# Kernel optimization log

Hardware: AMD Instinct MI355X
Metric: run time of the kernel (lower is better)

Reference implementation:

```python
import jax, jax.numpy as jnp
import numpy as np

D = 1024
H = 16
DH = D // H

def setup_inputs() -> dict:
    key = jax.random.key(0)
    ks = jax.random.split(key, 9)
    s = 0.02
    return {
        "x": jax.random.normal(ks[0], (2, 2048, D), dtype=jnp.float32),
        "Wq": jax.random.normal(ks[1], (D, D), dtype=jnp.float32) * s,
        "bq": jnp.zeros((D,), dtype=jnp.float32),
        "Wk": jax.random.normal(ks[2], (D, D), dtype=jnp.float32) * s,
        "bk": jnp.zeros((D,), dtype=jnp.float32),
        "Wv": jax.random.normal(ks[3], (D, D), dtype=jnp.float32) * s,
        "bv": jnp.zeros((D,), dtype=jnp.float32),
        "Wo": jax.random.normal(ks[4], (D, D), dtype=jnp.float32) * s,
        "bo": jnp.zeros((D,), dtype=jnp.float32),
    }

def reference(x, Wq, bq, Wk, bk, Wv, bv, Wo, bo):
    B, S, Dm = x.shape
    def proj(W, b):
        # [B,S,D] -> [B,H,S,DH]
        return (x @ W + b).reshape(B, S, H, DH).transpose(0, 2, 1, 3)
    q = proj(Wq, bq)
    k = proj(Wk, bk)
    v = proj(Wv, bv)
    scale = 1.0 / np.sqrt(DH).astype(np.float32)
    raw = jnp.einsum('bhsd,bhtd->bhst', q, k) * scale  # [B,H,S,S]
    w = jax.nn.softmax(raw, axis=-1)
    out = jnp.einsum('bhst,bhtd->bhsd', w, v)          # [B,H,S,DH]
    out = out.transpose(0, 2, 1, 3).reshape(B, S, Dm)
    return out @ Wo + bo
```

## Files before the change

### kernel.cpp

```cpp
#include <hip/hip_runtime.h>
#include <math.h>

constexpr int Dm  = 1024;
constexpr int NH  = 16;
constexpr int SQ  = 2048;
constexpr int NB  = 2;

typedef float f32x4 __attribute__((ext_vector_type(4)));
typedef float f32x16 __attribute__((ext_vector_type(16)));
typedef short bf16x8 __attribute__((ext_vector_type(8)));
typedef __attribute__((address_space(3))) unsigned int lds_u32;
typedef __attribute__((address_space(1))) const unsigned int glb_u32;

__device__ __forceinline__ void gload_lds16(const void* g, void* l) {
    __builtin_amdgcn_global_load_lds((glb_u32*)(uintptr_t)g, (lds_u32*)(uintptr_t)l, 16, 0, 0);
}

__device__ __forceinline__ unsigned short bf_round(float x) {
    unsigned u = __float_as_uint(x);
    unsigned r = u + 0x7fffu + ((u >> 16) & 1u);
    return (unsigned short)(r >> 16);
}

__device__ __forceinline__ float exp2_fast(float x) {
    float r;
    asm("v_exp_f32 %0, %1" : "=v"(r) : "v"(x));
    return r;
}

__device__ __forceinline__ unsigned cvt_pk(float lo, float hi_) {
    unsigned r;
    asm("v_cvt_pk_bf16_f32 %0, %1, %2" : "=v"(r) : "v"(lo), "v"(hi_));
    return r;
}

__device__ __forceinline__ void permlane_swap(unsigned& a, unsigned& b) {
    asm volatile("v_permlane32_swap_b32 %0, %1" : "+v"(a), "+v"(b));
}

__device__ __forceinline__ bf16x8 make_frag(unsigned a, unsigned b, unsigned c, unsigned d) {
    union { unsigned u[4]; bf16x8 v; } uu;
    uu.u[0] = a; uu.u[1] = b; uu.u[2] = c; uu.u[3] = d;
    return uu.v;
}

__global__ __launch_bounds__(256) void prologue(const float* __restrict__ x,
                                                const float* __restrict__ Wq,
                                                const float* __restrict__ Wk,
                                                const float* __restrict__ Wv,
                                                const float* __restrict__ Wo,
                                                unsigned short* __restrict__ xb,
                                                unsigned short* __restrict__ wt) {
    const int z = blockIdx.z;
    const int tid = threadIdx.x;
    if (z == 4) {
        size_t base = ((size_t)blockIdx.y * 16 + blockIdx.x) * 16384;
#pragma unroll
        for (int it = 0; it < 8; ++it) {
            size_t i = base + (size_t)it * 2048 + (size_t)tid * 8;
            float4 a = *(const float4*)&x[i];
            float4 b = *(const float4*)&x[i + 4];
            unsigned short o8[8] __attribute__((aligned(16)));
            o8[0] = bf_round(a.x); o8[1] = bf_round(a.y); o8[2] = bf_round(a.z); o8[3] = bf_round(a.w);
            o8[4] = bf_round(b.x); o8[5] = bf_round(b.y); o8[6] = bf_round(b.z); o8[7] = bf_round(b.w);
            *(uint4*)&xb[i] = *(const uint4*)o8;
        }
        return;
    }
    const float* W = (z == 0) ? Wq : (z == 1) ? Wk : (z == 2) ? Wv : Wo;
    unsigned short* dst = wt + (size_t)z * Dm * Dm;
    __shared__ float T[64][65];
    const int k0 = blockIdx.x * 64, n0 = blockIdx.y * 64;
#pragma unroll
    for (int i = 0; i < 4; ++i) {
        int s = tid + i * 256;
        int kk = s >> 4, c = (s & 15) * 4;
        *(float4*)&T[kk][c] = *(const float4*)&W[(size_t)(k0 + kk) * Dm + n0 + c];
    }
    __syncthreads();
#pragma unroll
    for (int i = 0; i < 2; ++i) {
        int s = tid + i * 256;
        int n = s >> 3, c8 = (s & 7) * 8;
        unsigned short o8[8] __attribute__((aligned(16)));
#pragma unroll
        for (int j = 0; j < 8; ++j) o8[j] = bf_round(T[c8 + j][n]);
        *(uint4*)&dst[(size_t)(n0 + n) * Dm + k0 + c8] = *(const uint4*)o8;
    }
}

__global__ __launch_bounds__(512) void gemm_qkv192(
    const unsigned short* __restrict__ xb,
    const unsigned short* __restrict__ wt,
    const float* __restrict__ bq, const float* __restrict__ bk,
    const float* __restrict__ bv,
    unsigned short* __restrict__ qbuf, unsigned short* __restrict__ kbuf,
    unsigned short* __restrict__ vtbuf)
{
    __shared__ unsigned short Alds[2][256 * 64];
    __shared__ unsigned short Blds[2][192 * 64];

    const int tid = threadIdx.x;
    const int lane = tid & 63, wid = tid >> 6;
    const int wm = wid >> 2, wn = wid & 3;
    const int l15 = lane & 15, lg = lane >> 4;

    const int bid = blockIdx.x;
    const int swz = (bid & 7) * 32 + (bid >> 3);
    const int bx = swz & 15, by = swz >> 4;
    const int m0 = by * 256, n0 = bx * 192;

    const int srow = wid * 8 + (lane >> 3);
    const int scol = ((lane & 7) ^ ((lane >> 3) & 7)) * 8;

    const unsigned short* Abase = xb + (size_t)m0 * Dm;
    const unsigned short* Bbase = wt + (size_t)n0 * Dm;

#define STAGE_TILE(t)                                                              \
    do {                                                                           \
        const unsigned short* As_ = Abase + (t) * 64;                              \
        const unsigned short* Bs_ = Bbase + (t) * 64;                              \
        unsigned short* Ad_ = Alds[(t) & 1];                                       \
        unsigned short* Bd_ = Blds[(t) & 1];                                       \
        _Pragma("unroll")                                                          \
        for (int i_ = 0; i_ < 4; ++i_)                                             \
            gload_lds16(&As_[(size_t)(i_ * 64 + srow) * Dm + scol],                \
                        &Ad_[i_ * 4096 + wid * 512]);                              \
        _Pragma("unroll")                                                          \
        for (int i_ = 0; i_ < 3; ++i_)                                             \
            gload_lds16(&Bs_[(size_t)(i_ * 64 + srow) * Dm + scol],                \
                        &Bd_[i_ * 4096 + wid * 512]);                              \
    } while (0)

    f32x4 acc[8][3];
#pragma unroll
    for (int mr = 0; mr < 8; ++mr)
#pragma unroll
        for (int nr = 0; nr < 3; ++nr) acc[mr][nr] = (f32x4){0.f, 0.f, 0.f, 0.f};

    STAGE_TILE(0);
    asm volatile("s_waitcnt vmcnt(0)" ::: "memory");
    __builtin_amdgcn_s_barrier();

    for (int t = 0; t < Dm / 64; ++t) {
        unsigned short* Ad = Alds[t & 1];
        unsigned short* Bd = Blds[t & 1];
        if (t + 1 < Dm / 64) STAGE_TILE(t + 1);

        bf16x8 a_[4][2], b_[3][2];

#define RD_A(qm, fr, ks) \
    (*(const bf16x8*)&Ad[(wm * 128 + (qm) * 64 + (fr) * 16 + l15) * 64 + \
                         ((((ks) * 4 + lg) ^ (l15 & 7)) * 8)])
#define RD_B(fc, ks) \
    (*(const bf16x8*)&Bd[(wn * 48 + (fc) * 16 + l15) * 64 + \
                         ((((ks) * 4 + lg) ^ (l15 & 7)) * 8)])

#pragma unroll
        for (int fr = 0; fr < 4; ++fr) {
            a_[fr][0] = RD_A(0, fr, 0); a_[fr][1] = RD_A(0, fr, 1);
        }
#pragma unroll
        for (int fc = 0; fc < 3; ++fc) {
            b_[fc][0] = RD_B(fc, 0); b_[fc][1] = RD_B(fc, 1);
        }
        __builtin_amdgcn_s_barrier();
        __builtin_amdgcn_s_setprio(1);
#pragma unroll
        for (int fr = 0; fr < 4; ++fr)
#pragma unroll
            for (int fc = 0; fc < 3; ++fc)
#pragma unroll
                for (int ks = 0; ks < 2; ++ks)
                    acc[fr][fc] = __builtin_amdgcn_mfma_f32_16x16x32_bf16(
                        a_[fr][ks], b_[fc][ks], acc[fr][fc], 0, 0, 0);
        __builtin_amdgcn_s_setprio(0);
        __builtin_amdgcn_s_barrier();

#pragma unroll
        for (int fr = 0; fr < 4; ++fr) {
            a_[fr][0] = RD_A(1, fr, 0); a_[fr][1] = RD_A(1, fr, 1);
        }
        __builtin_amdgcn_s_barrier();
        __builtin_amdgcn_s_setprio(1);
#pragma unroll
        for (int fr = 0; fr < 4; ++fr)
#pragma unroll
            for (int fc = 0; fc < 3; ++fc)
#pragma unroll
                for (int ks = 0; ks < 2; ++ks)
                    acc[4 + fr][fc] = __builtin_amdgcn_mfma_f32_16x16x32_bf16(
                        a_[fr][ks], b_[fc][ks], acc[4 + fr][fc], 0, 0, 0);
        __builtin_amdgcn_s_setprio(0);
        __builtin_amdgcn_s_barrier();

        asm volatile("s_waitcnt vmcnt(0)" ::: "memory");
        __builtin_amdgcn_s_barrier();
#undef RD_A
#undef RD_B
    }

    const float qscale = 0.18033688011f;
#pragma unroll
    for (int mr = 0; mr < 8; ++mr) {
#pragma unroll
        for (int nr = 0; nr < 3; ++nr) {
            const int m = m0 + wm * 128 + mr * 16 + lg * 4;
            const int nglob = n0 + wn * 48 + nr * 16 + l15;
            const int zq = nglob >> 10;
            const int nz = nglob & 1023;
            const float* bias = (zq == 0) ? bq : (zq == 1) ? bk : bv;
            const float bb_ = bias[nz];
            if (zq == 0) {
#pragma unroll
                for (int rr = 0; rr < 4; ++rr)
                    qbuf[(size_t)(m + rr) * Dm + nz] =
                        bf_round((acc[mr][nr][rr] + bb_) * qscale);
            } else if (zq == 1) {
#pragma unroll
                for (int rr = 0; rr < 4; ++rr)
                    kbuf[(size_t)(m + rr) * Dm + nz] = bf_round(acc[mr][nr][rr] + bb_);
            } else {
                const int bbv = m >> 11, s = m & (SQ - 1);
                const int hh = nz >> 6, d = nz & 63;
                unsigned short p4[4] __attribute__((aligned(8)));
#pragma unroll
                for (int rr = 0; rr < 4; ++rr) p4[rr] = bf_round(acc[mr][nr][rr] + bb_);
                *(uint2*)&vtbuf[(((size_t)bbv * NH + hh) * 64 + d) * SQ + s] =
                    *(const uint2*)p4;
            }
        }
    }
#undef STAGE_TILE
}

__global__ __launch_bounds__(256) void gemm_out8(const unsigned short* __restrict__ A,
                                                 const unsigned short* __restrict__ Bt,
                                                 const float* __restrict__ bias,
                                                 float* __restrict__ Cf) {
    __shared__ unsigned short Alds[2][128 * 64];
    __shared__ unsigned short Blds[2][128 * 64];

    const int tid = threadIdx.x;
    const int lane = tid & 63, wid = tid >> 6;
    const int l15 = lane & 15, lg = lane >> 4;
    const int wr = (wid >> 1) * 64, wc = (wid & 1) * 64;
    const int m0 = blockIdx.y * 128, n0 = blockIdx.x * 128;

    const int srow = (tid >> 3) & 31;
    const int scol = ((tid & 7) ^ (srow & 7)) * 8;

    const unsigned short* Abase = A + (size_t)m0 * Dm;
    const unsigned short* Bbase = Bt + (size_t)n0 * Dm;

#define STAGE_TILE(t)                                                              \
    do {                                                                           \
        const unsigned short* As_ = Abase + (t) * 64;                              \
        const unsigned short* Bs_ = Bbase + (t) * 64;                              \
        unsigned short* Ad_ = Alds[(t) & 1];                                       \
        unsigned short* Bd_ = Blds[(t) & 1];                                       \
        _Pragma("unroll")                                                          \
        for (int i_ = 0; i_ < 4; ++i_) {                                           \
            gload_lds16(&As_[(size_t)(i_ * 32 + srow) * Dm + scol],                \
                        &Ad_[i_ * 2048 + wid * 512]);                              \
            gload_lds16(&Bs_[(size_t)(i_ * 32 + srow) * Dm + scol],                \
                        &Bd_[i_ * 2048 + wid * 512]);                              \
        }                                                                          \
    } while (0)

    f32x4 acc[4][4];
#pragma unroll
    for (int r = 0; r < 4; ++r)
#pragma unroll
        for (int c = 0; c < 4; ++c) acc[r][c] = (f32x4){0.f, 0.f, 0.f, 0.f};

    STAGE_TILE(0);
    asm volatile("s_waitcnt vmcnt(0)" ::: "memory");
    __builtin_amdgcn_s_barrier();

    for (int t = 0; t < Dm / 64; ++t) {
        unsigned short* Ad = Alds[t & 1];
        unsigned short* Bd = Blds[t & 1];
        if (t + 1 < Dm / 64) STAGE_TILE(t + 1);

        bf16x8 a_[4][2], b_[2][2];

#define RD_A(fr, ks) \
    (*(const bf16x8*)&Ad[(wr + (fr) * 16 + l15) * 64 + ((((ks) * 4 + lg) ^ (l15 & 7)) * 8)])
#define RD_B(fc, ks) \
    (*(const bf16x8*)&Bd[(wc + (fc) * 16 + l15) * 64 + ((((ks) * 4 + lg) ^ (l15 & 7)) * 8)])

#pragma unroll
        for (int fr = 0; fr < 4; ++fr) {
            a_[fr][0] = RD_A(fr, 0); a_[fr][1] = RD_A(fr, 1);
        }
#pragma unroll
        for (int fc = 0; fc < 2; ++fc) {
            b_[fc][0] = RD_B(fc, 0); b_[fc][1] = RD_B(fc, 1);
        }
        __builtin_amdgcn_s_barrier();
        __builtin_amdgcn_s_setprio(1);
#pragma unroll
        for (int fr = 0; fr < 4; ++fr)
#pragma unroll
            for (int fc = 0; fc < 2; ++fc)
#pragma unroll
                for (int ks = 0; ks < 2; ++ks)
                    acc[fr][fc] = __builtin_amdgcn_mfma_f32_16x16x32_bf16(
                        a_[fr][ks], b_[fc][ks], acc[fr][fc], 0, 0, 0);
        __builtin_amdgcn_s_setprio(0);
        __builtin_amdgcn_s_barrier();

#pragma unroll
        for (int fc = 0; fc < 2; ++fc) {
            b_[fc][0] = RD_B(2 + fc, 0); b_[fc][1] = RD_B(2 + fc, 1);
        }
        __builtin_amdgcn_s_barrier();
        __builtin_amdgcn_s_setprio(1);
#pragma unroll
        for (int fr = 0; fr < 4; ++fr)
#pragma unroll
            for (int fc = 0; fc < 2; ++fc)
#pragma unroll
                for (int ks = 0; ks < 2; ++ks)
                    acc[fr][2 + fc] = __builtin_amdgcn_mfma_f32_16x16x32_bf16(
                        a_[fr][ks], b_[fc][ks], acc[fr][2 + fc], 0, 0, 0);
        __builtin_amdgcn_s_setprio(0);
        __builtin_amdgcn_s_barrier();

        asm volatile("s_waitcnt vmcnt(0)" ::: "memory");
        __builtin_amdgcn_s_barrier();
#undef RD_A
#undef RD_B
    }

#pragma unroll
    for (int r = 0; r < 4; ++r) {
#pragma unroll
        for (int c = 0; c < 4; ++c) {
            const int mBase = m0 + wr + r * 16 + lg * 4;
            const int n = n0 + wc + c * 16 + l15;
            const float bv_ = bias[n];
#pragma unroll
            for (int rr = 0; rr < 4; ++rr)
                Cf[(size_t)(mBase + rr) * Dm + n] = acc[r][c][rr] + bv_;
        }
    }
#undef STAGE_TILE
}

__global__ __launch_bounds__(256) void attn_bf16(const unsigned short* q,
                                                 const unsigned short* __restrict__ k,
                                                 const unsigned short* __restrict__ vt,
                                                 unsigned short* ao) {
    __shared__ unsigned short KVs[2][2][64 * 64];
    const int qt = blockIdx.x, h = blockIdx.y, b = blockIdx.z;
    const int tid = threadIdx.x, lane = tid & 63, wid = tid >> 6;
    const int l31 = lane & 31, hi = lane >> 5;

    const size_t qrow0 = (size_t)b * SQ + qt * 128;
    const unsigned short* qp = q + (qrow0 + wid * 32 + l31) * Dm + h * 64;
    bf16x8 qf[4];
#pragma unroll
    for (int ks = 0; ks < 4; ++ks)
        qf[ks] = *(const bf16x8*)&qp[ks * 16 + hi * 8];

    const unsigned short* kb = k + (size_t)b * SQ * Dm + h * 64;
    const unsigned short* vb = vt + ((size_t)b * NH + h) * 64 * SQ;

    const int row0 = tid >> 3;
    const int s8 = (tid & 7) * 8;
    const int sw8 = (((tid & 7) ^ (row0 & 7))) * 8;
    const int koff0 = row0 * 64 + sw8;
    const int koff1 = (row0 + 32) * 64 + sw8;

    {
        uint4 k0v = *(const uint4*)&kb[(size_t)row0 * Dm + s8];
        uint4 k1v = *(const uint4*)&kb[(size_t)(row0 + 32) * Dm + s8];
        uint4 v0v = *(const uint4*)&vb[(size_t)row0 * SQ + s8];
        uint4 v1v = *(const uint4*)&vb[(size_t)(row0 + 32) * SQ + s8];
        *(uint4*)&KVs[0][0][koff0] = k0v; *(uint4*)&KVs[0][0][koff1] = k1v;
        *(uint4*)&KVs[0][1][koff0] = v0v; *(uint4*)&KVs[0][1][koff1] = v1v;
    }
    __syncthreads();

    float psum = 0.f;
    f32x16 c0, c1;
#pragma unroll
    for (int i = 0; i < 16; ++i) { c0[i] = 0.f; c1[i] = 0.f; }

    int cur = 0;
    for (int t0 = 0; t0 < SQ; t0 += 64) {
        const bool hasNext = (t0 + 64) < SQ;
        uint4 kr0, kr1, vr0, vr1;
        if (hasNext) {
            const unsigned short* kn = kb + (size_t)(t0 + 64) * Dm;
            const unsigned short* vn = vb + (t0 + 64);
            kr0 = *(const uint4*)&kn[(size_t)row0 * Dm + s8];
            kr1 = *(const uint4*)&kn[(size_t)(row0 + 32) * Dm + s8];
            vr0 = *(const uint4*)&vn[(size_t)row0 * SQ + s8];
            vr1 = *(const uint4*)&vn[(size_t)(row0 + 32) * SQ + s8];
        }
        const unsigned short* Kc = KVs[cur][0];
        const unsigned short* Vc = KVs[cur][1];

#pragma unroll
        for (int kblk = 0; kblk < 2; ++kblk) {
            f32x16 p;
#pragma unroll
            for (int i = 0; i < 16; ++i) p[i] = 0.f;
            __builtin_amdgcn_s_setprio(1);
#pragma unroll
            for (int ks = 0; ks < 4; ++ks) {
                int row = kblk * 32 + l31;
                int slot = ((ks * 2 + hi) ^ (l31 & 7)) * 8;
                bf16x8 kf = *(const bf16x8*)&Kc[row * 64 + slot];
                p = __builtin_amdgcn_mfma_f32_32x32x16_bf16(kf, qf[ks], p, 0, 0, 0);
            }
            __builtin_amdgcn_s_setprio(0);

            float e[16];
#pragma unroll
            for (int i = 0; i < 16; ++i) { e[i] = exp2_fast(p[i]); psum += e[i]; }
            unsigned w0 = cvt_pk(e[0], e[1]),   w1 = cvt_pk(e[2], e[3]);
            unsigned w2 = cvt_pk(e[4], e[5]),   w3 = cvt_pk(e[6], e[7]);
            unsigned w4 = cvt_pk(e[8], e[9]),   w5 = cvt_pk(e[10], e[11]);
            unsigned w6 = cvt_pk(e[12], e[13]), w7 = cvt_pk(e[14], e[15]);
            permlane_swap(w0, w2); permlane_swap(w1, w3);
            permlane_swap(w4, w6); permlane_swap(w5, w7);
            bf16x8 pf0 = make_frag(w0, w1, w2, w3);
            bf16x8 pf1 = make_frag(w4, w5, w6, w7);

            int s0 = ((kblk * 4 + hi) ^ (l31 & 7)) * 8;
            int s1 = ((kblk * 4 + 2 + hi) ^ (l31 & 7)) * 8;
            bf16x8 va0 = *(const bf16x8*)&Vc[l31 * 64 + s0];
            bf16x8 va1 = *(const bf16x8*)&Vc[l31 * 64 + s1];
            bf16x8 vb0 = *(const bf16x8*)&Vc[(32 + l31) * 64 + s0];
            bf16x8 vb1 = *(const bf16x8*)&Vc[(32 + l31) * 64 + s1];
            __builtin_amdgcn_s_setprio(1);
            c0 = __builtin_amdgcn_mfma_f32_32x32x16_bf16(va0, pf0, c0, 0, 0, 0);
            c0 = __builtin_amdgcn_mfma_f32_32x32x16_bf16(va1, pf1, c0, 0, 0, 0);
            c1 = __builtin_amdgcn_mfma_f32_32x32x16_bf16(vb0, pf0, c1, 0, 0, 0);
            c1 = __builtin_amdgcn_mfma_f32_32x32x16_bf16(vb1, pf1, c1, 0, 0, 0);
            __builtin_amdgcn_s_setprio(0);
        }

        if (hasNext) {
            unsigned short* Kn = KVs[cur ^ 1][0];
            unsigned short* Vn = KVs[cur ^ 1][1];
            *(uint4*)&Kn[koff0] = kr0; *(uint4*)&Kn[koff1] = kr1;
            *(uint4*)&Vn[koff0] = vr0; *(uint4*)&Vn[koff1] = vr1;
        }
        __syncthreads();
        cur ^= 1;
    }

    float s = psum + __shfl_xor(psum, 32, 64);
    float inv = 1.f / s;

    unsigned short* Olds = (unsigned short*)KVs;
    {
        const int orow = wid * 32 + l31;
#pragma unroll
        for (int db = 0; db < 2; ++db) {
#pragma unroll
            for (int i = 0; i < 8; ++i) {
                float lo  = (db ? c1[2 * i] : c0[2 * i]) * inv;
                float hi_ = (db ? c1[2 * i + 1] : c0[2 * i + 1]) * inv;
                unsigned w = cvt_pk(lo, hi_);
                int d7 = hi * 4 + (i & 1) * 2;
                int slot = db * 4 + (i >> 1);
                int sw = slot ^ (l31 & 7);
                *(unsigned*)&Olds[orow * 64 + sw * 8 + d7] = w;
            }
        }
    }
    __syncthreads();
    {
        int r = tid >> 1, half = tid & 1;
        unsigned short* dst = ao + (qrow0 + r) * Dm + h * 64 + half * 32;
#pragma unroll
        for (int j = 0; j < 4; ++j) {
            int slot = half * 4 + j;
            int sw = slot ^ (r & 7);
            *(uint4*)&dst[j * 8] = *(const uint4*)&Olds[r * 64 + sw * 8];
        }
    }
}

extern "C" void kernel_launch(void* const* d_in, const int* in_sizes, int n_in,
                              void* d_out, int out_size, void* d_ws, size_t ws_size,
                              hipStream_t stream) {
    const float* x  = (const float*)d_in[0];
    const float* Wq = (const float*)d_in[1];
    const float* bq = (const float*)d_in[2];
    const float* Wk = (const float*)d_in[3];
    const float* bk = (const float*)d_in[4];
    const float* Wv = (const float*)d_in[5];
    const float* bv = (const float*)d_in[6];
    const float* Wo = (const float*)d_in[7];
    const float* bo = (const float*)d_in[8];
    float* out = (float*)d_out;

    const size_t M = (size_t)NB * SQ;
    const size_t elems = M * Dm;
    unsigned short* xb    = (unsigned short*)d_ws;
    unsigned short* wtb   = xb + elems;
    unsigned short* qbuf  = wtb + 4ull * Dm * Dm;
    unsigned short* kbuf  = qbuf + elems;
    unsigned short* vtbuf = kbuf + elems;

    dim3 blk(256);
    hipLaunchKernelGGL(prologue, dim3(16, 16, 5), blk, 0, stream,
                       x, Wq, Wk, Wv, Wo, xb, wtb);

    hipLaunchKernelGGL(gemm_qkv192, dim3(256), dim3(512), 0, stream,
                       xb, wtb, bq, bk, bv, qbuf, kbuf, vtbuf);

    hipLaunchKernelGGL(attn_bf16, dim3(SQ / 128, NH, NB), blk, 0, stream,
                       qbuf, kbuf, vtbuf, qbuf);

    hipLaunchKernelGGL(gemm_out8, dim3(Dm / 128, M / 128), blk, 0, stream,
                       qbuf, wtb + 3ull * Dm * Dm, bo, out);
}
```

Baseline: 113.7 us.

## Split attention over key halves and add a combine kernel

Splits each attention block's key range into two halves, launching twice as many blocks. Each block writes unnormalized bf16 partial outputs and row sums to workspace, and a new combine kernel adds them, normalizes and writes the head output. This raises the block count from 512 to 1024 to fill more compute units, at the cost of an extra launch, extra global traffic for the partials, and bf16 rounding of the partial sums. The split path is taken only when the workspace is large enough.

```diff
diff --git a/kernel.cpp b/kernel.cpp
--- a/kernel.cpp
+++ b/kernel.cpp
@@ -42,6 +42,10 @@
     union { unsigned u[4]; bf16x8 v; } uu;
     uu.u[0] = a; uu.u[1] = b; uu.u[2] = c; uu.u[3] = d;
     return uu.v;
+}
+
+__device__ __forceinline__ float bfu2f(unsigned lo16) {
+    return __uint_as_float(lo16 << 16);
 }
 
 __global__ __launch_bounds__(256) void prologue(const float* __restrict__ x,
@@ -349,12 +353,20 @@
 #undef STAGE_TILE
 }
 
-__global__ __launch_bounds__(256) void attn_bf16(const unsigned short* q,
+template <int SPLIT>
+__global__ __launch_bounds__(256) void attn_core(const unsigned short* q,
                                                  const unsigned short* __restrict__ k,
                                                  const unsigned short* __restrict__ vt,
-                                                 unsigned short* ao) {
+                                                 unsigned short* ao,
+                                                 unsigned* __restrict__ op0,
+                                                 unsigned* __restrict__ op1,
+                                                 float* __restrict__ ps0,
+                                                 float* __restrict__ ps1) {
     __shared__ unsigned short KVs[2][2][64 * 64];
-    const int qt = blockIdx.x, h = blockIdx.y, b = blockIdx.z;
+    const int qt = blockIdx.x, h = blockIdx.y;
+    const int bz = blockIdx.z;
+    const int b = SPLIT ? (bz >> 1) : bz;
+    const int half = SPLIT ? (bz & 1) : 0;
     const int tid = threadIdx.x, lane = tid & 63, wid = tid >> 6;
     const int l31 = lane & 31, hi = lane >> 5;
 
@@ -365,8 +377,8 @@
     for (int ks = 0; ks < 4; ++ks)
         qf[ks] = *(const bf16x8*)&qp[ks * 16 + hi * 8];
 
-    const unsigned short* kb = k + (size_t)b * SQ * Dm + h * 64;
-    const unsigned short* vb = vt + ((size_t)b * NH + h) * 64 * SQ;
+    const unsigned short* kb = k + ((size_t)b * SQ + half * (SQ / 2)) * Dm + h * 64;
+    const unsigned short* vb = vt + ((size_t)b * NH + h) * 64 * SQ + half * (SQ / 2);
 
     const int row0 = tid >> 3;
     const int s8 = (tid & 7) * 8;
@@ -389,9 +401,10 @@
 #pragma unroll
     for (int i = 0; i < 16; ++i) { c0[i] = 0.f; c1[i] = 0.f; }
 
+    const int NKEYS = SPLIT ? (SQ / 2) : SQ;
     int cur = 0;
-    for (int t0 = 0; t0 < SQ; t0 += 64) {
-        const bool hasNext = (t0 + 64) < SQ;
+    for (int t0 = 0; t0 < NKEYS; t0 += 64) {
+        const bool hasNext = (t0 + 64) < NKEYS;
         uint4 kr0, kr1, vr0, vr1;
         if (hasNext) {
             const unsigned short* kn = kb + (size_t)(t0 + 64) * Dm;
@@ -456,11 +469,26 @@
     }
 
     float s = psum + __shfl_xor(psum, 32, 64);
+    const int qloc = wid * 32 + l31;
+
+    if (SPLIT) {
+        unsigned* op = half ? op1 : op0;
+        float* ps = half ? ps1 : ps0;
+        const size_t pbase = (((size_t)b * NH + h) * (SQ / 128) + qt) * 128;
+        unsigned* ob = op + pbase * 32;
+#pragma unroll
+        for (int p = 0; p < 8; ++p) {
+            int dp = (p & 1) + 4 * (p >> 1) + 2 * hi;
+            ob[dp * 128 + qloc] = cvt_pk(c0[2 * p], c0[2 * p + 1]);
+            ob[(16 + dp) * 128 + qloc] = cvt_pk(c1[2 * p], c1[2 * p + 1]);
+        }
+        if (hi == 0) ps[pbase + qloc] = s;
+        return;
+    }
+
     float inv = 1.f / s;
-
     unsigned short* Olds = (unsigned short*)KVs;
     {
-        const int orow = wid * 32 + l31;
 #pragma unroll
         for (int db = 0; db < 2; ++db) {
 #pragma unroll
@@ -471,21 +499,48 @@
                 int d7 = hi * 4 + (i & 1) * 2;
                 int slot = db * 4 + (i >> 1);
                 int sw = slot ^ (l31 & 7);
-                *(unsigned*)&Olds[orow * 64 + sw * 8 + d7] = w;
+                *(unsigned*)&Olds[qloc * 64 + sw * 8 + d7] = w;
             }
         }
     }
     __syncthreads();
     {
-        int r = tid >> 1, half = tid & 1;
-        unsigned short* dst = ao + (qrow0 + r) * Dm + h * 64 + half * 32;
+        int r = tid >> 1, hf = tid & 1;
+        unsigned short* dst = ao + (qrow0 + r) * Dm + h * 64 + hf * 32;
 #pragma unroll
         for (int j = 0; j < 4; ++j) {
-            int slot = half * 4 + j;
+            int slot = hf * 4 + j;
             int sw = slot ^ (r & 7);
             *(uint4*)&dst[j * 8] = *(const uint4*)&Olds[r * 64 + sw * 8];
         }
     }
+}
+
+__global__ __launch_bounds__(128) void attn_combine(const unsigned* __restrict__ op0,
+                                                    const unsigned* __restrict__ op1,
+                                                    const float* __restrict__ ps0,
+                                                    const float* __restrict__ ps1,
+                                                    unsigned short* __restrict__ ao) {
+    const int qt = blockIdx.x, h = blockIdx.y, b = blockIdx.z;
+    const int tid = threadIdx.x;
+    const size_t pbase = (((size_t)b * NH + h) * (SQ / 128) + qt) * 128;
+    const float inv = 1.f / (ps0[pbase + tid] + ps1[pbase + tid]);
+    const unsigned* o0 = op0 + pbase * 32;
+    const unsigned* o1 = op1 + pbase * 32;
+
+    unsigned out[32] __attribute__((aligned(16)));
+#pragma unroll
+    for (int dp = 0; dp < 32; ++dp) {
+        unsigned u0 = o0[dp * 128 + tid];
+        unsigned u1 = o1[dp * 128 + tid];
+        float lo = (bfu2f(u0 & 0xffffu) + bfu2f(u1 & 0xffffu)) * inv;
+        float hi = (bfu2f(u0 >> 16) + bfu2f(u1 >> 16)) * inv;
+        out[dp] = cvt_pk(lo, hi);
+    }
+    unsigned short* dst = ao + ((size_t)b * SQ + qt * 128 + tid) * Dm + h * 64;
+#pragma unroll
+    for (int j = 0; j < 8; ++j)
+        *(uint4*)&dst[j * 8] = *(const uint4*)&out[j * 4];
 }
 
 extern "C" void kernel_launch(void* const* d_in, const int* in_sizes, int n_in,
@@ -509,6 +564,12 @@
     unsigned short* qbuf  = wtb + 4ull * Dm * Dm;
     unsigned short* kbuf  = qbuf + elems;
     unsigned short* vtbuf = kbuf + elems;
+    unsigned* op0 = (unsigned*)xb;
+    unsigned* op1 = (unsigned*)(vtbuf + elems);
+    float* ps0 = (float*)(op1 + 2ull * 1024 * 1024);
+    float* ps1 = ps0 + 65536;
+    const size_t need = (size_t)((char*)(ps1 + 65536) - (char*)d_ws);
+    const bool use_split = ws_size >= need;
 
     dim3 blk(256);
     hipLaunchKernelGGL(prologue, dim3(16, 16, 5), blk, 0, stream,
@@ -517,8 +578,15 @@
     hipLaunchKernelGGL(gemm_qkv192, dim3(256), dim3(512), 0, stream,
                        xb, wtb, bq, bk, bv, qbuf, kbuf, vtbuf);
 
-    hipLaunchKernelGGL(attn_bf16, dim3(SQ / 128, NH, NB), blk, 0, stream,
-                       qbuf, kbuf, vtbuf, qbuf);
+    if (use_split) {
+        hipLaunchKernelGGL(attn_core<1>, dim3(SQ / 128, NH, NB * 2), blk, 0, stream,
+                           qbuf, kbuf, vtbuf, qbuf, op0, op1, ps0, ps1);
+        hipLaunchKernelGGL(attn_combine, dim3(SQ / 128, NH, NB), dim3(128), 0, stream,
+                           op0, op1, ps0, ps1, qbuf);
+    } else {
+        hipLaunchKernelGGL(attn_core<0>, dim3(SQ / 128, NH, NB), blk, 0, stream,
+                           qbuf, kbuf, vtbuf, qbuf, op0, op1, ps0, ps1);
+    }
 
     hipLaunchKernelGGL(gemm_out8, dim3(Dm / 128, M / 128), blk, 0, stream,
                        qbuf, wtb + 3ull * Dm * Dm, bo, out);
```

After: 122.8 us. +8.0%, slower.
